# Optimization experiments

Measured on AMD Instinct MI355X. Metric: run time of the kernel, lower is better.

The kernel has to match this reference:

```python
import jax, jax.numpy as jnp
import numpy as np

TRACT_SPECS = [
    dict(name="x_a", src_size=4096, dst_size=1024, connections=64, seed=42),
    dict(name="x_b", src_size=4096, dst_size=512, connections=64, seed=43),
    dict(name="x_c", src_size=2048, dst_size=512, connections=32, seed=44),
]


def _make_mask(dst_size, src_size, n_conn, seed):
    rng = np.random.RandomState(seed)
    mask = np.zeros((dst_size, src_size), dtype=np.float32)
    for dst in range(dst_size):
        idx = rng.choice(src_size, size=min(n_conn, src_size), replace=False)
        mask[dst, idx] = 1.0
    return jnp.asarray(mask)


def _xavier_uniform(key, dst, src):
    # matches nn.init.xavier_uniform_ for a (dst, src) weight
    limit = float(np.sqrt(6.0 / (dst + src)))
    return jax.random.uniform(key, (dst, src), jnp.float32, -limit, limit)


def setup_inputs() -> dict:
    key = jax.random.key(0)
    keys = jax.random.split(key, 6)
    B, S = 8, 1024
    inp = {}
    for i, spec in enumerate(TRACT_SPECS):
        src, dst = spec["src_size"], spec["dst_size"]
        inp[spec["name"]] = jax.random.normal(keys[i], (B, S, src), jnp.float32)
        inp["w_" + spec["name"][-1]] = _xavier_uniform(keys[3 + i], dst, src)
        inp["m_" + spec["name"][-1]] = _make_mask(dst, src, spec["connections"], spec["seed"])
    return inp


def reference(x_a, x_b, x_c, w_a, w_b, w_c, m_a, m_b, m_c):
    # Each tract: F.linear(x, weight * mask) -> x @ (W*M)^T; then concat on last dim.
    out_a = jnp.einsum("bsi,oi->bso", x_a, w_a * m_a)
    out_b = jnp.einsum("bsi,oi->bso", x_b, w_b * m_b)
    out_c = jnp.einsum("bsi,oi->bso", x_c, w_c * m_c)
    return jnp.concatenate([out_a, out_b, out_c], axis=-1)
```

## Files before the change

### kernel.cpp

```cpp
#include <hip/hip_runtime.h>
#include <hip/hip_fp16.h>
#include <stdint.h>


#define BS_TOTAL 8192
#define SRC_A 4096
#define SRC_B 4096
#define SRC_C 2048
#define DST_A 1024
#define DST_B 512
#define DST_C 512
#define K_A 64
#define K_B 64
#define K_C 32
#define OUT_DIM 2048
#define ROWS 4

#define NBLK_A (BS_TOTAL / ROWS)
#define NBLK_B (BS_TOTAL / ROWS)
#define NBLK_C (BS_TOTAL / ROWS)
#define LDS_BYTES (SRC_A * 8)

typedef float f32x4 __attribute__((ext_vector_type(4)));


__global__ __launch_bounds__(256) void compress_kernel(
    const float* __restrict__ w_a, const float* __restrict__ m_a,
    const float* __restrict__ w_b, const float* __restrict__ m_b,
    const float* __restrict__ w_c, const float* __restrict__ m_c,
    unsigned* __restrict__ pa, unsigned* __restrict__ pb,
    unsigned* __restrict__ pc) {
    __shared__ int s_cnt;
    __shared__ int s_idx[64];
    __shared__ int s_bankcnt[16];
    __shared__ int s_bankoff[16];
    __shared__ unsigned s_sorted[64];

    const int blk = blockIdx.x;
    const int t = threadIdx.x;

    const float *w, *m;
    unsigned* p;
    int dst, src_n, K, DST;
    if (blk < DST_A) {
        w = w_a; m = m_a; p = pa; dst = blk;
        src_n = SRC_A; K = K_A; DST = DST_A;
    } else if (blk < DST_A + DST_B) {
        w = w_b; m = m_b; p = pb; dst = blk - DST_A;
        src_n = SRC_B; K = K_B; DST = DST_B;
    } else {
        w = w_c; m = m_c; p = pc; dst = blk - DST_A - DST_B;
        src_n = SRC_C; K = K_C; DST = DST_C;
    }

    if (t == 0) s_cnt = 0;
    if (t < 16) s_bankcnt[t] = 0;
    __syncthreads();

    const float* mrow = m + (size_t)dst * src_n;
    const float* wrow = w + (size_t)dst * src_n;
    const f32x4* m4 = (const f32x4*)mrow;
    const int nq = src_n >> 10;
    for (int i = 0; i < nq; ++i) {
        int q = t + (i << 8);
        f32x4 mv = m4[q];
#pragma unroll
        for (int j = 0; j < 4; ++j) {
            if (mv[j] != 0.0f) {
                int pos = atomicAdd(&s_cnt, 1);
                if (pos < 64) s_idx[pos] = 4 * q + j;
            }
        }
    }
    __syncthreads();
    int cnt = s_cnt;
    if (cnt > K) cnt = K;

    if (t < cnt) atomicAdd(&s_bankcnt[s_idx[t] & 15], 1);
    __syncthreads();
    if (t == 0) {
        int acc = 0;
        for (int b = 0; b < 16; ++b) {
            s_bankoff[b] = acc;
            acc += s_bankcnt[b];
        }
    }
    __syncthreads();
    if (t < cnt) {
        int idx = s_idx[t];
        int j = atomicAdd(&s_bankoff[idx & 15], 1);
        float wv = wrow[idx] * mrow[idx];
        unsigned hb = (unsigned)__half_as_ushort(__float2half(wv));
        s_sorted[j] = ((unsigned)idx << 16) | hb;
    }
    __syncthreads();
    if (t >= cnt && t < K) s_sorted[t] = 0u;
    __syncthreads();

    if (t < K) {
        int rot = (K == 64) ? ((dst & 15) << 2) : ((dst & 15) << 1);
        unsigned v = s_sorted[(t + rot) & (K - 1)];
        p[(((t >> 2) * DST) + dst) * 4 + (t & 3)] = v;
    }
}


#define PROC(u) {                                                            \
        uint2 xv = xp[(u) >> 16];                                            \
        float w = __half2float(__ushort_as_half((unsigned short)((u) & 0xffffu))); \
        const __half2 hlo = *(const __half2*)&xv.x;                          \
        const __half2 hhi = *(const __half2*)&xv.y;                          \
        acc0 = fmaf(w, __low2float(hlo), acc0);                              \
        acc1 = fmaf(w, __high2float(hlo), acc1);                             \
        acc2 = fmaf(w, __low2float(hhi), acc2);                              \
        acc3 = fmaf(w, __high2float(hhi), acc3); }

template <int SRCN, int KQ, int DSTN, int NOUT>
__device__ __forceinline__ void do_tract(
    const float* __restrict__ xsrc, const uint4* __restrict__ tab,
    float* __restrict__ outb,
    size_t r0, int t, unsigned* xs) {
    const f32x4* s0 = (const f32x4*)(xsrc + (r0 + 0) * SRCN);
    const f32x4* s1 = (const f32x4*)(xsrc + (r0 + 1) * SRCN);
    const f32x4* s2 = (const f32x4*)(xsrc + (r0 + 2) * SRCN);
    const f32x4* s3 = (const f32x4*)(xsrc + (r0 + 3) * SRCN);
    uint4* xs4 = (uint4*)xs;

#pragma unroll
    for (int i = 0; i < (SRCN >> 10); ++i) {
        int q = t + (i << 8);
        f32x4 v0 = s0[q];
        f32x4 v1 = s1[q];
        f32x4 v2 = s2[q];
        f32x4 v3 = s3[q];
        uint4 w0, w1;
        __half2 h;
        h = __floats2half2_rn(v0.x, v1.x); w0.x = *(unsigned*)&h;
        h = __floats2half2_rn(v2.x, v3.x); w0.y = *(unsigned*)&h;
        h = __floats2half2_rn(v0.y, v1.y); w0.z = *(unsigned*)&h;
        h = __floats2half2_rn(v2.y, v3.y); w0.w = *(unsigned*)&h;
        h = __floats2half2_rn(v0.z, v1.z); w1.x = *(unsigned*)&h;
        h = __floats2half2_rn(v2.z, v3.z); w1.y = *(unsigned*)&h;
        h = __floats2half2_rn(v0.w, v1.w); w1.z = *(unsigned*)&h;
        h = __floats2half2_rn(v2.w, v3.w); w1.w = *(unsigned*)&h;
        xs4[2 * q]     = w0;
        xs4[2 * q + 1] = w1;
    }
    __syncthreads();

    const uint2* xp = (const uint2*)xs;
    float* o0 = outb;
    float* o1 = outb + OUT_DIM;
    float* o2 = outb + 2 * OUT_DIM;
    float* o3 = outb + 3 * OUT_DIM;

#pragma unroll 1
    for (int o = 0; o < NOUT; ++o) {
        int dst = t + (o << 8);
        float acc0 = 0.0f, acc1 = 0.0f, acc2 = 0.0f, acc3 = 0.0f;
#pragma unroll
        for (int k4 = 0; k4 < KQ; ++k4) {
            uint4 e = tab[k4 * DSTN + dst];
            PROC(e.x) PROC(e.y) PROC(e.z) PROC(e.w)
        }
        __builtin_nontemporal_store(acc0, o0 + dst);
        __builtin_nontemporal_store(acc1, o1 + dst);
        __builtin_nontemporal_store(acc2, o2 + dst);
        __builtin_nontemporal_store(acc3, o3 + dst);
    }
}

__global__ __launch_bounds__(256) void tract_kernel(
    const float* __restrict__ x_a, const float* __restrict__ x_b,
    const float* __restrict__ x_c,
    const unsigned* __restrict__ pa, const unsigned* __restrict__ pb,
    const unsigned* __restrict__ pc,
    float* __restrict__ out) {
    extern __shared__ unsigned xs[];
    const int t = threadIdx.x;
    const int blk = blockIdx.x;

    if (blk < NBLK_A) {
        size_t r0 = (size_t)blk * ROWS;
        do_tract<SRC_A, K_A / 4, DST_A, 4>(
            x_a, (const uint4*)pa, out + r0 * OUT_DIM, r0, t, xs);
    } else if (blk < NBLK_A + NBLK_B) {
        size_t r0 = (size_t)(blk - NBLK_A) * ROWS;
        do_tract<SRC_B, K_B / 4, DST_B, 2>(
            x_b, (const uint4*)pb, out + r0 * OUT_DIM + DST_A, r0, t, xs);
    } else {
        size_t r0 = (size_t)(blk - NBLK_A - NBLK_B) * ROWS;
        do_tract<SRC_C, K_C / 4, DST_C, 2>(
            x_c, (const uint4*)pc, out + r0 * OUT_DIM + DST_A + DST_B, r0, t, xs);
    }
}

extern "C" void kernel_launch(void* const* d_in, const int* in_sizes, int n_in,
                              void* d_out, int out_size, void* d_ws, size_t ws_size,
                              hipStream_t stream) {
    const float* x_a = (const float*)d_in[0];
    const float* w_a = (const float*)d_in[1];
    const float* m_a = (const float*)d_in[2];
    const float* x_b = (const float*)d_in[3];
    const float* w_b = (const float*)d_in[4];
    const float* m_b = (const float*)d_in[5];
    const float* x_c = (const float*)d_in[6];
    const float* w_c = (const float*)d_in[7];
    const float* m_c = (const float*)d_in[8];
    float* out = (float*)d_out;

    char* ws = (char*)d_ws;
    unsigned* pa = (unsigned*)(ws);
    unsigned* pb = (unsigned*)(ws + 262144);
    unsigned* pc = (unsigned*)(ws + 262144 + 131072);

    compress_kernel<<<DST_A + DST_B + DST_C, 256, 0, stream>>>(
        w_a, m_a, w_b, m_b, w_c, m_c, pa, pb, pc);
    tract_kernel<<<NBLK_A + NBLK_B + NBLK_C, 256, LDS_BYTES, stream>>>(
        x_a, x_b, x_c, pa, pb, pc, out);
}
```

Baseline: 380.9 us.

## Process eight rows per block with 16-byte LDS records and 512 threads

```diff
diff --git a/kernel.cpp b/kernel.cpp
--- a/kernel.cpp
+++ b/kernel.cpp
@@ -14,12 +14,11 @@
 #define K_B 64
 #define K_C 32
 #define OUT_DIM 2048
-#define ROWS 4
-
-#define NBLK_A (BS_TOTAL / ROWS)
-#define NBLK_B (BS_TOTAL / ROWS)
-#define NBLK_C (BS_TOTAL / ROWS)
-#define LDS_BYTES (SRC_A * 8)
+#define ROWS 8
+#define THREADS 512
+
+#define NBLK (BS_TOTAL / ROWS)
+#define LDS_BYTES (SRC_A * 16)
 
 typedef float f32x4 __attribute__((ext_vector_type(4)));
 
@@ -32,8 +31,8 @@
     unsigned* __restrict__ pc) {
     __shared__ int s_cnt;
     __shared__ int s_idx[64];
-    __shared__ int s_bankcnt[16];
-    __shared__ int s_bankoff[16];
+    __shared__ int s_bankcnt[8];
+    __shared__ int s_bankoff[8];
     __shared__ unsigned s_sorted[64];
 
     const int blk = blockIdx.x;
@@ -54,7 +53,7 @@
     }
 
     if (t == 0) s_cnt = 0;
-    if (t < 16) s_bankcnt[t] = 0;
+    if (t < 8) s_bankcnt[t] = 0;
     __syncthreads();
 
     const float* mrow = m + (size_t)dst * src_n;
@@ -76,11 +75,11 @@
     int cnt = s_cnt;
     if (cnt > K) cnt = K;
 
-    if (t < cnt) atomicAdd(&s_bankcnt[s_idx[t] & 15], 1);
+    if (t < cnt) atomicAdd(&s_bankcnt[s_idx[t] & 7], 1);
     __syncthreads();
     if (t == 0) {
         int acc = 0;
-        for (int b = 0; b < 16; ++b) {
+        for (int b = 0; b < 8; ++b) {
             s_bankoff[b] = acc;
             acc += s_bankcnt[b];
         }
@@ -88,17 +87,17 @@
     __syncthreads();
     if (t < cnt) {
         int idx = s_idx[t];
-        int j = atomicAdd(&s_bankoff[idx & 15], 1);
+        int j = atomicAdd(&s_bankoff[idx & 7], 1);
         float wv = wrow[idx] * mrow[idx];
         unsigned hb = (unsigned)__half_as_ushort(__float2half(wv));
-        s_sorted[j] = ((unsigned)idx << 16) | hb;
+        s_sorted[j] = ((unsigned)(idx << 4) << 16) | hb;
     }
     __syncthreads();
     if (t >= cnt && t < K) s_sorted[t] = 0u;
     __syncthreads();
 
     if (t < K) {
-        int rot = (K == 64) ? ((dst & 15) << 2) : ((dst & 15) << 1);
+        int rot = (K == 64) ? ((dst & 7) << 3) : ((dst & 7) << 2);
         unsigned v = s_sorted[(t + rot) & (K - 1)];
         p[(((t >> 2) * DST) + dst) * 4 + (t & 3)] = v;
     }
@@ -106,14 +105,20 @@
 
 
 #define PROC(u) {                                                            \
-        uint2 xv = xp[(u) >> 16];                                            \
+        const uint4 xv = *(const uint4*)((const char*)xs + ((u) >> 16));     \
         float w = __half2float(__ushort_as_half((unsigned short)((u) & 0xffffu))); \
-        const __half2 hlo = *(const __half2*)&xv.x;                          \
-        const __half2 hhi = *(const __half2*)&xv.y;                          \
-        acc0 = fmaf(w, __low2float(hlo), acc0);                              \
-        acc1 = fmaf(w, __high2float(hlo), acc1);                             \
-        acc2 = fmaf(w, __low2float(hhi), acc2);                              \
-        acc3 = fmaf(w, __high2float(hhi), acc3); }
+        const __half2 h01 = *(const __half2*)&xv.x;                          \
+        const __half2 h23 = *(const __half2*)&xv.y;                          \
+        const __half2 h45 = *(const __half2*)&xv.z;                          \
+        const __half2 h67 = *(const __half2*)&xv.w;                          \
+        acc0 = fmaf(w, __low2float(h01), acc0);                              \
+        acc1 = fmaf(w, __high2float(h01), acc1);                             \
+        acc2 = fmaf(w, __low2float(h23), acc2);                              \
+        acc3 = fmaf(w, __high2float(h23), acc3);                             \
+        acc4 = fmaf(w, __low2float(h45), acc4);                              \
+        acc5 = fmaf(w, __high2float(h45), acc5);                             \
+        acc6 = fmaf(w, __low2float(h67), acc6);                              \
+        acc7 = fmaf(w, __high2float(h67), acc7); }
 
 template <int SRCN, int KQ, int DSTN, int NOUT>
 __device__ __forceinline__ void do_tract(
@@ -124,53 +129,60 @@
     const f32x4* s1 = (const f32x4*)(xsrc + (r0 + 1) * SRCN);
     const f32x4* s2 = (const f32x4*)(xsrc + (r0 + 2) * SRCN);
     const f32x4* s3 = (const f32x4*)(xsrc + (r0 + 3) * SRCN);
+    const f32x4* s4 = (const f32x4*)(xsrc + (r0 + 4) * SRCN);
+    const f32x4* s5 = (const f32x4*)(xsrc + (r0 + 5) * SRCN);
+    const f32x4* s6 = (const f32x4*)(xsrc + (r0 + 6) * SRCN);
+    const f32x4* s7 = (const f32x4*)(xsrc + (r0 + 7) * SRCN);
     uint4* xs4 = (uint4*)xs;
 
 #pragma unroll
-    for (int i = 0; i < (SRCN >> 10); ++i) {
-        int q = t + (i << 8);
+    for (int i = 0; i < (SRCN >> 11); ++i) {
+        int q = t + (i << 9);
         f32x4 v0 = s0[q];
         f32x4 v1 = s1[q];
         f32x4 v2 = s2[q];
         f32x4 v3 = s3[q];
-        uint4 w0, w1;
+        f32x4 v4 = s4[q];
+        f32x4 v5 = s5[q];
+        f32x4 v6 = s6[q];
+        f32x4 v7 = s7[q];
         __half2 h;
-        h = __floats2half2_rn(v0.x, v1.x); w0.x = *(unsigned*)&h;
-        h = __floats2half2_rn(v2.x, v3.x); w0.y = *(unsigned*)&h;
-        h = __floats2half2_rn(v0.y, v1.y); w0.z = *(unsigned*)&h;
-        h = __floats2half2_rn(v2.y, v3.y); w0.w = *(unsigned*)&h;
-        h = __floats2half2_rn(v0.z, v1.z); w1.x = *(unsigned*)&h;
-        h = __floats2half2_rn(v2.z, v3.z); w1.y = *(unsigned*)&h;
-        h = __floats2half2_rn(v0.w, v1.w); w1.z = *(unsigned*)&h;
-        h = __floats2half2_rn(v2.w, v3.w); w1.w = *(unsigned*)&h;
-        xs4[2 * q]     = w0;
-        xs4[2 * q + 1] = w1;
-    }
-    __syncthreads();
-
-    const uint2* xp = (const uint2*)xs;
+        uint4 rec;
+#pragma unroll
+        for (int j = 0; j < 4; ++j) {
+            h = __floats2half2_rn(v0[j], v1[j]); rec.x = *(unsigned*)&h;
+            h = __floats2half2_rn(v2[j], v3[j]); rec.y = *(unsigned*)&h;
+            h = __floats2half2_rn(v4[j], v5[j]); rec.z = *(unsigned*)&h;
+            h = __floats2half2_rn(v6[j], v7[j]); rec.w = *(unsigned*)&h;
+            xs4[4 * q + j] = rec;
+        }
+    }
+    __syncthreads();
+
     float* o0 = outb;
-    float* o1 = outb + OUT_DIM;
-    float* o2 = outb + 2 * OUT_DIM;
-    float* o3 = outb + 3 * OUT_DIM;
 
 #pragma unroll 1
     for (int o = 0; o < NOUT; ++o) {
-        int dst = t + (o << 8);
+        int dst = t + (o << 9);
         float acc0 = 0.0f, acc1 = 0.0f, acc2 = 0.0f, acc3 = 0.0f;
-#pragma unroll
+        float acc4 = 0.0f, acc5 = 0.0f, acc6 = 0.0f, acc7 = 0.0f;
+#pragma unroll 4
         for (int k4 = 0; k4 < KQ; ++k4) {
             uint4 e = tab[k4 * DSTN + dst];
             PROC(e.x) PROC(e.y) PROC(e.z) PROC(e.w)
         }
-        __builtin_nontemporal_store(acc0, o0 + dst);
-        __builtin_nontemporal_store(acc1, o1 + dst);
-        __builtin_nontemporal_store(acc2, o2 + dst);
-        __builtin_nontemporal_store(acc3, o3 + dst);
-    }
-}
-
-__global__ __launch_bounds__(256) void tract_kernel(
+        __builtin_nontemporal_store(acc0, o0 + 0 * OUT_DIM + dst);
+        __builtin_nontemporal_store(acc1, o0 + 1 * OUT_DIM + dst);
+        __builtin_nontemporal_store(acc2, o0 + 2 * OUT_DIM + dst);
+        __builtin_nontemporal_store(acc3, o0 + 3 * OUT_DIM + dst);
+        __builtin_nontemporal_store(acc4, o0 + 4 * OUT_DIM + dst);
+        __builtin_nontemporal_store(acc5, o0 + 5 * OUT_DIM + dst);
+        __builtin_nontemporal_store(acc6, o0 + 6 * OUT_DIM + dst);
+        __builtin_nontemporal_store(acc7, o0 + 7 * OUT_DIM + dst);
+    }
+}
+
+__global__ __launch_bounds__(THREADS, 4) void tract_kernel(
     const float* __restrict__ x_a, const float* __restrict__ x_b,
     const float* __restrict__ x_c,
     const unsigned* __restrict__ pa, const unsigned* __restrict__ pb,
@@ -180,17 +192,17 @@
     const int t = threadIdx.x;
     const int blk = blockIdx.x;
 
-    if (blk < NBLK_A) {
+    if (blk < NBLK) {
         size_t r0 = (size_t)blk * ROWS;
-        do_tract<SRC_A, K_A / 4, DST_A, 4>(
+        do_tract<SRC_A, K_A / 4, DST_A, 2>(
             x_a, (const uint4*)pa, out + r0 * OUT_DIM, r0, t, xs);
-    } else if (blk < NBLK_A + NBLK_B) {
-        size_t r0 = (size_t)(blk - NBLK_A) * ROWS;
-        do_tract<SRC_B, K_B / 4, DST_B, 2>(
+    } else if (blk < 2 * NBLK) {
+        size_t r0 = (size_t)(blk - NBLK) * ROWS;
+        do_tract<SRC_B, K_B / 4, DST_B, 1>(
             x_b, (const uint4*)pb, out + r0 * OUT_DIM + DST_A, r0, t, xs);
     } else {
-        size_t r0 = (size_t)(blk - NBLK_A - NBLK_B) * ROWS;
-        do_tract<SRC_C, K_C / 4, DST_C, 2>(
+        size_t r0 = (size_t)(blk - 2 * NBLK) * ROWS;
+        do_tract<SRC_C, K_C / 4, DST_C, 1>(
             x_c, (const uint4*)pc, out + r0 * OUT_DIM + DST_A + DST_B, r0, t, xs);
     }
 }
@@ -214,8 +226,15 @@
     unsigned* pb = (unsigned*)(ws + 262144);
     unsigned* pc = (unsigned*)(ws + 262144 + 131072);
 
+    static bool configured = false;
+    if (!configured) {
+        hipFuncSetAttribute(reinterpret_cast<const void*>(&tract_kernel),
+                            hipFuncAttributeMaxDynamicSharedMemorySize, LDS_BYTES);
+        configured = true;
+    }
+
     compress_kernel<<<DST_A + DST_B + DST_C, 256, 0, stream>>>(
         w_a, m_a, w_b, m_b, w_c, m_c, pa, pb, pc);
-    tract_kernel<<<NBLK_A + NBLK_B + NBLK_C, 256, LDS_BYTES, stream>>>(
+    tract_kernel<<<3 * NBLK, THREADS, LDS_BYTES, stream>>>(
         x_a, x_b, x_c, pa, pb, pc, out);
 }
```

Result: slower. 403.2 us (+5.9%).

## Swizzle LDS activation layout and process two outputs per thread iteration

Applied to the files above, without the earlier changes.

```diff
diff --git a/kernel.cpp b/kernel.cpp
--- a/kernel.cpp
+++ b/kernel.cpp
@@ -15,10 +15,7 @@
 #define K_C 32
 #define OUT_DIM 2048
 #define ROWS 4
-
-#define NBLK_A (BS_TOTAL / ROWS)
-#define NBLK_B (BS_TOTAL / ROWS)
-#define NBLK_C (BS_TOTAL / ROWS)
+#define NBLK (BS_TOTAL / ROWS)
 #define LDS_BYTES (SRC_A * 8)
 
 typedef float f32x4 __attribute__((ext_vector_type(4)));
@@ -76,7 +73,13 @@
     int cnt = s_cnt;
     if (cnt > K) cnt = K;
 
-    if (t < cnt) atomicAdd(&s_bankcnt[s_idx[t] & 15], 1);
+    if (t < cnt) {
+        int idx = s_idx[t];
+        unsigned u = (unsigned)idx >> 1;
+        unsigned up = u ^ ((u >> 3) & 7u);
+        int key = (int)(((up & 7u) << 1) | ((unsigned)idx & 1u));
+        atomicAdd(&s_bankcnt[key], 1);
+    }
     __syncthreads();
     if (t == 0) {
         int acc = 0;
@@ -88,10 +91,14 @@
     __syncthreads();
     if (t < cnt) {
         int idx = s_idx[t];
-        int j = atomicAdd(&s_bankoff[idx & 15], 1);
+        unsigned u = (unsigned)idx >> 1;
+        unsigned up = u ^ ((u >> 3) & 7u);
+        unsigned boff = (up << 4) | (((unsigned)idx & 1u) << 3);
+        int key = (int)(((up & 7u) << 1) | ((unsigned)idx & 1u));
+        int j = atomicAdd(&s_bankoff[key], 1);
         float wv = wrow[idx] * mrow[idx];
         unsigned hb = (unsigned)__half_as_ushort(__float2half(wv));
-        s_sorted[j] = ((unsigned)idx << 16) | hb;
+        s_sorted[j] = (boff << 16) | hb;
     }
     __syncthreads();
     if (t >= cnt && t < K) s_sorted[t] = 0u;
@@ -105,17 +112,17 @@
 }
 
 
-#define PROC(u) {                                                            \
-        uint2 xv = xp[(u) >> 16];                                            \
-        float w = __half2float(__ushort_as_half((unsigned short)((u) & 0xffffu))); \
+#define PROC(u, A0, A1, A2, A3) {                                            \
+        const uint2 xv = *(const uint2*)((const char*)xs + ((u) >> 16));     \
+        const float w = __half2float(__ushort_as_half((unsigned short)((u) & 0xffffu))); \
         const __half2 hlo = *(const __half2*)&xv.x;                          \
         const __half2 hhi = *(const __half2*)&xv.y;                          \
-        acc0 = fmaf(w, __low2float(hlo), acc0);                              \
-        acc1 = fmaf(w, __high2float(hlo), acc1);                             \
-        acc2 = fmaf(w, __low2float(hhi), acc2);                              \
-        acc3 = fmaf(w, __high2float(hhi), acc3); }
-
-template <int SRCN, int KQ, int DSTN, int NOUT>
+        A0 = fmaf(w, __low2float(hlo), A0);                                  \
+        A1 = fmaf(w, __high2float(hlo), A1);                                 \
+        A2 = fmaf(w, __low2float(hhi), A2);                                  \
+        A3 = fmaf(w, __high2float(hhi), A3); }
+
+template <int SRCN, int KQ, int DSTN, int NPAIR>
 __device__ __forceinline__ void do_tract(
     const float* __restrict__ xsrc, const uint4* __restrict__ tab,
     float* __restrict__ outb,
@@ -143,30 +150,39 @@
         h = __floats2half2_rn(v2.z, v3.z); w1.y = *(unsigned*)&h;
         h = __floats2half2_rn(v0.w, v1.w); w1.z = *(unsigned*)&h;
         h = __floats2half2_rn(v2.w, v3.w); w1.w = *(unsigned*)&h;
-        xs4[2 * q]     = w0;
-        xs4[2 * q + 1] = w1;
-    }
-    __syncthreads();
-
-    const uint2* xp = (const uint2*)xs;
-    float* o0 = outb;
-    float* o1 = outb + OUT_DIM;
-    float* o2 = outb + 2 * OUT_DIM;
-    float* o3 = outb + 3 * OUT_DIM;
+        unsigned u0 = (unsigned)(2 * q);
+        unsigned up0 = u0 ^ ((u0 >> 3) & 7u);
+        xs4[up0]     = w0;
+        xs4[up0 ^ 1] = w1;
+    }
+    __syncthreads();
 
 #pragma unroll 1
-    for (int o = 0; o < NOUT; ++o) {
-        int dst = t + (o << 8);
-        float acc0 = 0.0f, acc1 = 0.0f, acc2 = 0.0f, acc3 = 0.0f;
-#pragma unroll
+    for (int op = 0; op < NPAIR; ++op) {
+        const int d0 = t + (op << 9);
+        float a0 = 0.f, a1 = 0.f, a2 = 0.f, a3 = 0.f;
+        float b0 = 0.f, b1 = 0.f, b2 = 0.f, b3 = 0.f;
+#pragma unroll 4
         for (int k4 = 0; k4 < KQ; ++k4) {
-            uint4 e = tab[k4 * DSTN + dst];
-            PROC(e.x) PROC(e.y) PROC(e.z) PROC(e.w)
+            uint4 e0 = tab[k4 * DSTN + d0];
+            uint4 e1 = tab[k4 * DSTN + d0 + 256];
+            PROC(e0.x, a0, a1, a2, a3)
+            PROC(e1.x, b0, b1, b2, b3)
+            PROC(e0.y, a0, a1, a2, a3)
+            PROC(e1.y, b0, b1, b2, b3)
+            PROC(e0.z, a0, a1, a2, a3)
+            PROC(e1.z, b0, b1, b2, b3)
+            PROC(e0.w, a0, a1, a2, a3)
+            PROC(e1.w, b0, b1, b2, b3)
         }
-        __builtin_nontemporal_store(acc0, o0 + dst);
-        __builtin_nontemporal_store(acc1, o1 + dst);
-        __builtin_nontemporal_store(acc2, o2 + dst);
-        __builtin_nontemporal_store(acc3, o3 + dst);
+        __builtin_nontemporal_store(a0, outb + 0 * OUT_DIM + d0);
+        __builtin_nontemporal_store(a1, outb + 1 * OUT_DIM + d0);
+        __builtin_nontemporal_store(a2, outb + 2 * OUT_DIM + d0);
+        __builtin_nontemporal_store(a3, outb + 3 * OUT_DIM + d0);
+        __builtin_nontemporal_store(b0, outb + 0 * OUT_DIM + d0 + 256);
+        __builtin_nontemporal_store(b1, outb + 1 * OUT_DIM + d0 + 256);
+        __builtin_nontemporal_store(b2, outb + 2 * OUT_DIM + d0 + 256);
+        __builtin_nontemporal_store(b3, outb + 3 * OUT_DIM + d0 + 256);
     }
 }
 
@@ -180,17 +196,17 @@
     const int t = threadIdx.x;
     const int blk = blockIdx.x;
 
-    if (blk < NBLK_A) {
+    if (blk < NBLK) {
         size_t r0 = (size_t)blk * ROWS;
-        do_tract<SRC_A, K_A / 4, DST_A, 4>(
+        do_tract<SRC_A, K_A / 4, DST_A, 2>(
             x_a, (const uint4*)pa, out + r0 * OUT_DIM, r0, t, xs);
-    } else if (blk < NBLK_A + NBLK_B) {
-        size_t r0 = (size_t)(blk - NBLK_A) * ROWS;
-        do_tract<SRC_B, K_B / 4, DST_B, 2>(
+    } else if (blk < 2 * NBLK) {
+        size_t r0 = (size_t)(blk - NBLK) * ROWS;
+        do_tract<SRC_B, K_B / 4, DST_B, 1>(
             x_b, (const uint4*)pb, out + r0 * OUT_DIM + DST_A, r0, t, xs);
     } else {
-        size_t r0 = (size_t)(blk - NBLK_A - NBLK_B) * ROWS;
-        do_tract<SRC_C, K_C / 4, DST_C, 2>(
+        size_t r0 = (size_t)(blk - 2 * NBLK) * ROWS;
+        do_tract<SRC_C, K_C / 4, DST_C, 1>(
             x_c, (const uint4*)pc, out + r0 * OUT_DIM + DST_A + DST_B, r0, t, xs);
     }
 }
@@ -216,6 +232,6 @@
 
     compress_kernel<<<DST_A + DST_B + DST_C, 256, 0, stream>>>(
         w_a, m_a, w_b, m_b, w_c, m_c, pa, pb, pc);
-    tract_kernel<<<NBLK_A + NBLK_B + NBLK_C, 256, LDS_BYTES, stream>>>(
+    tract_kernel<<<3 * NBLK, 256, LDS_BYTES, stream>>>(
         x_a, x_b, x_c, pa, pb, pc, out);
 }
```

New measurement: 389.9 us. 2.4% more time.
